# Kernel optimization log

Measured on AMD Instinct MI355X. Metric: run time of the kernel, lower is better.

Reference implementation:

```python
import jax, jax.numpy as jnp
import numpy as np

H = 256
L = 2048
OPINION_LIST = jnp.array([19, 20, 21, 33, 34, 35, 41, 42, 43, 44, 45, 46])


def setup_inputs() -> dict:
    key = jax.random.key(0)
    ks = jax.random.split(key, 8)
    B = 8
    opinion_features = jax.random.normal(ks[0], (B, L, H), dtype=jnp.float32)
    text_features = jax.random.normal(ks[1], (B, L, H), dtype=jnp.float32)
    pos_ids = jax.random.randint(ks[2], (B, L), 0, 47)
    scale = 1.0 / np.sqrt(H)
    Wt = jax.random.normal(ks[3], (H, H), dtype=jnp.float32) * scale
    bt = jax.random.normal(ks[4], (H,), dtype=jnp.float32) * scale
    Wo = jax.random.normal(ks[5], (H, H), dtype=jnp.float32) * scale
    wa = jax.random.normal(ks[6], (2 * H,), dtype=jnp.float32) * scale
    ba = jax.random.normal(ks[7], (1,), dtype=jnp.float32) * scale
    return {"opinion_features": opinion_features, "text_features": text_features,
            "pos_ids": pos_ids, "Wt": Wt, "bt": bt, "Wo": Wo, "wa": wa, "ba": ba}


def position_bias(pos_ids):
    # base: 0.5 on diagonal, 1/log2(2+|i-j|) elsewhere  -> (L, L)
    idx = jnp.arange(L)
    dist = jnp.abs(idx[:, None] - idx[None, :]).astype(jnp.float32)
    base = jnp.where(dist == 0, 0.5, 1.0 / jnp.log2(2.0 + dist))
    # per-token column multiplier: 8 if POS tag is an opinion tag else 1 -> (B, L)
    is_op = (pos_ids[..., None] == OPINION_LIST).any(-1)
    mult = jnp.where(is_op, 8.0, 1.0).astype(jnp.float32)
    return base[None, :, :] * mult[:, None, :]  # (B, L, L)


def reference(opinion_features, text_features, pos_ids, Wt, bt, Wo, wa, ba):
    pos_m = position_bias(pos_ids)                      # (B, L, L)
    t = text_features @ Wt.T + bt                       # (B, L, H)
    o = opinion_features @ Wo.T                         # (B, L, H)
    # tanh(concat([t_i, o_j])) @ wa + ba decomposes additively since tanh is elementwise
    st = jnp.tanh(t) @ wa[:H]                           # (B, L)
    so = jnp.tanh(o) @ wa[H:]                           # (B, L)
    scores = (st[:, :, None] + so[:, None, :] + ba[0]) * pos_m  # (B, L, L)
    att = jax.nn.softmax(scores, axis=-1)
    return att @ opinion_features                       # (B, L, H)
```

## Files before the change

kernel.cpp:

```cpp
#include <hip/hip_runtime.h>

#define B_ 8
#define L_ 2048
#define H_ 256

typedef _Float16 half8 __attribute__((ext_vector_type(8)));
typedef _Float16 half4_t __attribute__((ext_vector_type(4)));
typedef float f32x4 __attribute__((ext_vector_type(4)));

__device__ __forceinline__ float fast_tanh(float x) {
    const float e2 = __expf(2.f * x);
    return 1.f - 2.f * __builtin_amdgcn_rcpf(e2 + 1.f);
}

__global__ __launch_bounds__(256, 2) void prep_kernel(
    const float* __restrict__ opin, const float* __restrict__ text,
    const int* __restrict__ pos_ids,
    const float* __restrict__ Wt, const float* __restrict__ bt,
    const float* __restrict__ Wo, const float* __restrict__ wa,
    const float* __restrict__ ba,
    float* __restrict__ ws_st, float2* __restrict__ ws_cm,
    _Float16* __restrict__ vtg)
{
    __shared__ __align__(16) _Float16 a_lds[4][8][512];
    __shared__ __align__(16) _Float16 w_lds[16][512];

    const int tid  = threadIdx.x;
    const int lane = tid & 63;
    const int rg   = tid >> 6;
    const int mat  = blockIdx.x & 1;
    const size_t g0 = (size_t)(blockIdx.x >> 1) * 64;

    const float* __restrict__ src = mat ? opin : text;
    const float* __restrict__ W   = mat ? Wo   : Wt;

    for (int v = 0; v < 16; ++v) {
        const int idx = v * 256 + tid;
        const int row = idx >> 6;
        const int k   = (idx & 63) * 4;
        const float4 f = *(const float4*)(src + (g0 + row) * 256 + k);
        half4_t h = { (_Float16)f.x, (_Float16)f.y, (_Float16)f.z, (_Float16)f.w };
        const int off = ((row & 15) + 16 * ((k >> 3) & 3)) * 8 + (k & 7);
        *(half4_t*)&a_lds[row >> 4][k >> 5][off] = h;
    }
    __syncthreads();

    f32x4 acc[16];
#pragma unroll
    for (int nt = 0; nt < 16; ++nt) acc[nt] = (f32x4){0.f, 0.f, 0.f, 0.f};

    for (int kc = 0; kc < 8; ++kc) {
        for (int p = 0; p < 8; ++p) {
            const int n = p * 32 + (tid >> 3);
            const int k = (tid & 7) * 4;
            const float4 f = *(const float4*)(W + n * 256 + kc * 32 + k);
            half4_t h = { (_Float16)f.x, (_Float16)f.y, (_Float16)f.z, (_Float16)f.w };
            const int off = ((n & 15) + 16 * (k >> 3)) * 8 + (k & 7);
            *(half4_t*)&w_lds[n >> 4][off] = h;
        }
        __syncthreads();
        const half8 afrag = *(const half8*)&a_lds[rg][kc][lane * 8];
#pragma unroll
        for (int nt = 0; nt < 16; ++nt) {
            const half8 bfrag = *(const half8*)&w_lds[nt][lane * 8];
            acc[nt] = __builtin_amdgcn_mfma_f32_16x16x32_f16(afrag, bfrag, acc[nt], 0, 0, 0);
        }
        __syncthreads();
    }

    const int em = lane & 15, q = lane >> 4;
    float rowsum[4] = {0.f, 0.f, 0.f, 0.f};
#pragma unroll
    for (int nt = 0; nt < 16; ++nt) {
        const int col  = nt * 16 + em;
        const float btv = mat ? 0.f : bt[col];
        const float wav = wa[mat * 256 + col];
#pragma unroll
        for (int r = 0; r < 4; ++r)
            rowsum[r] += fast_tanh(acc[nt][r] + btv) * wav;
    }
#pragma unroll
    for (int r = 0; r < 4; ++r) {
        float s = rowsum[r];
        s += __shfl_xor(s, 1, 64);
        s += __shfl_xor(s, 2, 64);
        s += __shfl_xor(s, 4, 64);
        s += __shfl_xor(s, 8, 64);
        if (em == 0) {
            const size_t grow = g0 + rg * 16 + q * 4 + r;
            if (mat == 0) {
                ws_st[grow] = s;
            } else {
                const int p = pos_ids[grow];
                const bool isop = (p==19)|(p==20)|(p==21)|(p==33)|(p==34)|(p==35)|((p>=41)&(p<=46));
                const float mult = isop ? 8.f : 1.f;
                const float c = s + ba[0];
                ws_cm[grow] = make_float2(c * mult, mult);
            }
        }
    }

    if (mat == 1) {
        const int h = tid;
        const size_t b = g0 >> 11;
        const int kcj = (int)((g0 & 2047) >> 6);
        const int kc = h >> 5, kq = (h >> 3) & 3, jh = h & 7;
        _Float16 vals[64];
#pragma unroll
        for (int r = 0; r < 64; ++r)
            vals[r] = a_lds[r >> 4][kc][((r & 15) + 16 * kq) * 8 + jh];
        _Float16* dst = vtg + ((size_t)b * 32 + kcj) * 16384 + h * 8;
#pragma unroll
        for (int w = 0; w < 8; ++w)
            *(half8*)(dst + w * 2048) = *(half8*)&vals[w * 8];
    }
}

__global__ __launch_bounds__(256, 2) void attn_kernel(
    const float* __restrict__ ws_st, const float2* __restrict__ ws_cm,
    const _Float16* __restrict__ vtg, float* __restrict__ out)
{
    __shared__ float t_lds[2048];
    __shared__ __align__(16) _Float16 p_lds[2][2][2][512];
    __shared__ __align__(16) float alpha_lds[2][32];
    __shared__ float z_lds[32];

    const int tid  = threadIdx.x;
    const int lane = tid & 63;
    const int hq   = tid >> 6;
    const int em   = lane & 15;
    const int q4   = lane >> 4;

    const int b  = blockIdx.x & 7;
    const int i0 = (blockIdx.x >> 3) * 32;

    const int row = tid >> 3;
    const int jg  = tid & 7;
    const int gi  = i0 + row;

#pragma unroll
    for (int v = 0; v < 8; ++v) {
        const int d = tid * 8 + v;
        const float bv = (d == 0) ? 0.5f : 1.0f / __log2f(2.f + (float)d);
        t_lds[d] = bv * 1.44269504088896f;
    }

    const float sti = ws_st[b * 2048 + gi];
    const _Float16* __restrict__ vb =
        vtg + ((size_t)b * 32) * 16384 + q4 * 2048 + (hq * 64 + em) * 8;

    f32x4 acc[2][4];
#pragma unroll
    for (int rt = 0; rt < 2; ++rt)
#pragma unroll
        for (int ht = 0; ht < 4; ++ht) acc[rt][ht] = (f32x4){0.f, 0.f, 0.f, 0.f};
    float m_run = -1e30f;
    float zacc  = 0.f;

    f32x4 vbuf[2][4];
#pragma unroll
    for (int ks = 0; ks < 2; ++ks)
#pragma unroll
        for (int ht = 0; ht < 4; ++ht)
            asm volatile("global_load_dwordx4 %0, %1, off"
                         : "=v"(vbuf[ks][ht])
                         : "v"(vb + ks * 8192 + ht * 128));

    __syncthreads();

    for (int kc = 0; kc < 32; ++kc) {
        const int j0  = kc * 64;
        const int buf = kc & 1;

        float s_arr[8];
        float mx = -1e30f;
        {
            const float4* __restrict__ cmp =
                (const float4*)(ws_cm + b * 2048 + j0 + jg * 8);
#pragma unroll
            for (int w = 0; w < 4; ++w) {
                const float4 c4 = cmp[w];
                const int jj = j0 + jg * 8 + w * 2;
                int d0 = gi - jj;     d0 = d0 < 0 ? -d0 : d0;
                int d1 = gi - jj - 1; d1 = d1 < 0 ? -d1 : d1;
                const float s0 = (sti * c4.y + c4.x) * t_lds[d0];
                const float s1 = (sti * c4.w + c4.z) * t_lds[d1];
                s_arr[2 * w]     = s0;
                s_arr[2 * w + 1] = s1;
                mx = fmaxf(mx, fmaxf(s0, s1));
            }
        }
        mx = fmaxf(mx, __shfl_xor(mx, 1, 64));
        mx = fmaxf(mx, __shfl_xor(mx, 2, 64));
        mx = fmaxf(mx, __shfl_xor(mx, 4, 64));

        const float m_new = fmaxf(m_run, mx);
        const float alpha = __builtin_amdgcn_exp2f(m_run - m_new);
        float zl = 0.f;
        half8 pv;
#pragma unroll
        for (int v = 0; v < 8; ++v) {
            const float p = __builtin_amdgcn_exp2f(s_arr[v] - m_new);
            zl += p;
            pv[v] = (_Float16)p;
        }
        zacc  = zacc * alpha + zl;
        m_run = m_new;

        {
            const int kq = jg & 3;
            const int slot = (((row & 15) ^ (kq << 1)) + 16 * kq);
            *(half8*)&p_lds[buf][row >> 4][jg >> 2][slot * 8] = pv;
        }
        if (jg == 0) alpha_lds[buf][row] = alpha;

        __syncthreads();

        {
            const float4 a0 = *(const float4*)&alpha_lds[buf][q4 * 4];
            const float4 a1 = *(const float4*)&alpha_lds[buf][16 + q4 * 4];
            float ar[2][4] = {{a0.x, a0.y, a0.z, a0.w}, {a1.x, a1.y, a1.z, a1.w}};
            bool upd = false;
#pragma unroll
            for (int rt = 0; rt < 2; ++rt)
#pragma unroll
                for (int r = 0; r < 4; ++r) upd |= (ar[rt][r] != 1.f);
            if (__any(upd)) {
#pragma unroll
                for (int rt = 0; rt < 2; ++rt)
#pragma unroll
                    for (int ht = 0; ht < 4; ++ht)
#pragma unroll
                        for (int r = 0; r < 4; ++r)
                            acc[rt][ht][r] *= ar[rt][r];
            }
        }

        asm volatile("s_waitcnt vmcnt(0)" ::: "memory");
        __builtin_amdgcn_sched_barrier(0);

        {
            const int sl8 = ((em ^ (q4 << 1)) + 16 * q4) * 8;
#pragma unroll
            for (int ks = 0; ks < 2; ++ks) {
                const half8 a0 = *(const half8*)&p_lds[buf][0][ks][sl8];
                const half8 a1 = *(const half8*)&p_lds[buf][1][ks][sl8];
#pragma unroll
                for (int ht = 0; ht < 4; ++ht) {
                    const half8 bh = __builtin_bit_cast(half8, vbuf[ks][ht]);
                    acc[0][ht] = __builtin_amdgcn_mfma_f32_16x16x32_f16(a0, bh, acc[0][ht], 0, 0, 0);
                    acc[1][ht] = __builtin_amdgcn_mfma_f32_16x16x32_f16(a1, bh, acc[1][ht], 0, 0, 0);
                }
            }
        }

        if (kc < 31) {
            const _Float16* __restrict__ pnext = vb + (size_t)(kc + 1) * 16384;
#pragma unroll
            for (int ks = 0; ks < 2; ++ks)
#pragma unroll
                for (int ht = 0; ht < 4; ++ht)
                    asm volatile("global_load_dwordx4 %0, %1, off"
                                 : "=v"(vbuf[ks][ht])
                                 : "v"(pnext + ks * 8192 + ht * 128));
        }
    }

    zacc += __shfl_xor(zacc, 1, 64);
    zacc += __shfl_xor(zacc, 2, 64);
    zacc += __shfl_xor(zacc, 4, 64);
    if (jg == 0) z_lds[row] = zacc;
    __syncthreads();

#pragma unroll
    for (int rt = 0; rt < 2; ++rt) {
#pragma unroll
        for (int r = 0; r < 4; ++r) {
            const int orow = rt * 16 + q4 * 4 + r;
            const float rz = 1.f / z_lds[orow];
#pragma unroll
            for (int ht = 0; ht < 4; ++ht)
                out[((size_t)b * 2048 + i0 + orow) * 256 + hq * 64 + ht * 16 + em] =
                    acc[rt][ht][r] * rz;
        }
    }
}

extern "C" void kernel_launch(void* const* d_in, const int* in_sizes, int n_in,
                              void* d_out, int out_size, void* d_ws, size_t ws_size,
                              hipStream_t stream) {
    const float* opin  = (const float*)d_in[0];
    const float* text  = (const float*)d_in[1];
    const int* pos_ids = (const int*)d_in[2];
    const float* Wt    = (const float*)d_in[3];
    const float* bt    = (const float*)d_in[4];
    const float* Wo    = (const float*)d_in[5];
    const float* wa    = (const float*)d_in[6];
    const float* ba    = (const float*)d_in[7];
    float* out         = (float*)d_out;

    float*  ws_st = (float*)d_ws;
    float2* ws_cm = (float2*)((char*)d_ws + 65536);
    _Float16* vtg = (_Float16*)((char*)d_ws + 65536 + 131072);

    prep_kernel<<<512, 256, 0, stream>>>(opin, text, pos_ids, Wt, bt, Wo, wa, ba,
                                         ws_st, ws_cm, vtg);
    attn_kernel<<<512, 256, 0, stream>>>(ws_st, ws_cm, vtg, out);
}
```

Measured before the change: 150.7 us.

## Software-pipeline weight and V loads, stage cm in LDS, overlap scores with MFMA

In the prep kernel, the next weight K-chunk is prefetched into registers while the current one is converted and used, and the weight LDS buffer is doubled so one barrier per chunk is enough. In the attention kernel, the per-batch cm vector is loaded once into LDS instead of being read from global memory every chunk. The V tiles are double-buffered in registers, and the score/softmax computation for the next chunk is placed after the MFMAs of the current chunk, so global latency and score ALU work overlap with matrix math. The cost is more VGPRs and LDS per block, which could lower occupancy, and a wrapped prefetch past the last chunk that loads data it never uses.

```diff
diff --git a/kernel.cpp b/kernel.cpp
--- a/kernel.cpp
+++ b/kernel.cpp
@@ -12,6 +12,12 @@
     const float e2 = __expf(2.f * x);
     return 1.f - 2.f * __builtin_amdgcn_rcpf(e2 + 1.f);
 }
+
+#define PHASE_BARRIER() do {                                   \
+        asm volatile("s_waitcnt lgkmcnt(0)" ::: "memory");     \
+        __builtin_amdgcn_s_barrier();                          \
+        __builtin_amdgcn_sched_barrier(0);                     \
+    } while (0)
 
 __global__ __launch_bounds__(256, 2) void prep_kernel(
     const float* __restrict__ opin, const float* __restrict__ text,
@@ -23,7 +29,7 @@
     _Float16* __restrict__ vtg)
 {
     __shared__ __align__(16) _Float16 a_lds[4][8][512];
-    __shared__ __align__(16) _Float16 w_lds[16][512];
+    __shared__ __align__(16) _Float16 w_lds[2][16][512];
 
     const int tid  = threadIdx.x;
     const int lane = tid & 63;
@@ -33,6 +39,19 @@
 
     const float* __restrict__ src = mat ? opin : text;
     const float* __restrict__ W   = mat ? Wo   : Wt;
+
+    f32x4 wregA[8], wregB[8];
+#define ISSUE_W(DST, KC) do {                                                   \
+        _Pragma("unroll")                                                       \
+        for (int p = 0; p < 8; ++p) {                                           \
+            const float* p_ = W + (p * 32 + (tid >> 3)) * 256 + (KC) * 32 +     \
+                              (tid & 7) * 4;                                    \
+            asm volatile("global_load_dwordx4 %0, %1, off"                      \
+                         : "=v"(DST[p]) : "v"(p_));                             \
+        }                                                                       \
+    } while (0)
+
+    ISSUE_W(wregA, 0);
 
     for (int v = 0; v < 16; ++v) {
         const int idx = v * 256 + tid;
@@ -43,30 +62,38 @@
         const int off = ((row & 15) + 16 * ((k >> 3) & 3)) * 8 + (k & 7);
         *(half4_t*)&a_lds[row >> 4][k >> 5][off] = h;
     }
-    __syncthreads();
+    PHASE_BARRIER();
 
     f32x4 acc[16];
 #pragma unroll
     for (int nt = 0; nt < 16; ++nt) acc[nt] = (f32x4){0.f, 0.f, 0.f, 0.f};
 
-    for (int kc = 0; kc < 8; ++kc) {
+    auto wbody = [&](const int kc, f32x4 (&cur)[8], f32x4 (&nxt)[8]) {
+        asm volatile("s_waitcnt vmcnt(0)" ::: "memory");
+        __builtin_amdgcn_sched_barrier(0);
+        if (kc < 7) ISSUE_W(nxt, kc + 1);
+#pragma unroll
         for (int p = 0; p < 8; ++p) {
             const int n = p * 32 + (tid >> 3);
             const int k = (tid & 7) * 4;
-            const float4 f = *(const float4*)(W + n * 256 + kc * 32 + k);
+            const float4 f = __builtin_bit_cast(float4, cur[p]);
             half4_t h = { (_Float16)f.x, (_Float16)f.y, (_Float16)f.z, (_Float16)f.w };
             const int off = ((n & 15) + 16 * (k >> 3)) * 8 + (k & 7);
-            *(half4_t*)&w_lds[n >> 4][off] = h;
-        }
-        __syncthreads();
+            *(half4_t*)&w_lds[kc & 1][n >> 4][off] = h;
+        }
+        PHASE_BARRIER();
         const half8 afrag = *(const half8*)&a_lds[rg][kc][lane * 8];
 #pragma unroll
         for (int nt = 0; nt < 16; ++nt) {
-            const half8 bfrag = *(const half8*)&w_lds[nt][lane * 8];
+            const half8 bfrag = *(const half8*)&w_lds[kc & 1][nt][lane * 8];
             acc[nt] = __builtin_amdgcn_mfma_f32_16x16x32_f16(afrag, bfrag, acc[nt], 0, 0, 0);
         }
-        __syncthreads();
-    }
+    };
+    for (int kc = 0; kc < 8; kc += 2) {
+        wbody(kc,     wregA, wregB);
+        wbody(kc + 1, wregB, wregA);
+    }
+#undef ISSUE_W
 
     const int em = lane & 15, q = lane >> 4;
     float rowsum[4] = {0.f, 0.f, 0.f, 0.f};
@@ -121,6 +148,7 @@
     const _Float16* __restrict__ vtg, float* __restrict__ out)
 {
     __shared__ float t_lds[2048];
+    __shared__ float cm_lds[4096];
     __shared__ __align__(16) _Float16 p_lds[2][2][2][512];
     __shared__ __align__(16) float alpha_lds[2][32];
     __shared__ float z_lds[32];
@@ -138,16 +166,36 @@
     const int jg  = tid & 7;
     const int gi  = i0 + row;
 
+    const _Float16* __restrict__ vb =
+        vtg + ((size_t)b * 32) * 16384 + q4 * 2048 + (hq * 64 + em) * 8;
+
+    f32x4 vbA[2][4], vbB[2][4];
+#define ISSUE_VB(DST, KC) do {                                                  \
+        const _Float16* p_ = vb + (size_t)((KC) & 31) * 16384;                  \
+        _Pragma("unroll")                                                       \
+        for (int ks = 0; ks < 2; ++ks)                                          \
+        _Pragma("unroll")                                                       \
+        for (int ht = 0; ht < 4; ++ht)                                          \
+            asm volatile("global_load_dwordx4 %0, %1, off"                      \
+                         : "=v"(DST[ks][ht]) : "v"(p_ + ks * 8192 + ht * 128)); \
+    } while (0)
+
+    ISSUE_VB(vbA, 0);
+
 #pragma unroll
     for (int v = 0; v < 8; ++v) {
         const int d = tid * 8 + v;
         const float bv = (d == 0) ? 0.5f : 1.0f / __log2f(2.f + (float)d);
         t_lds[d] = bv * 1.44269504088896f;
     }
+#pragma unroll
+    for (int v = 0; v < 4; ++v) {
+        const int idx = (v * 256 + tid) * 4;
+        *(float4*)&cm_lds[idx] =
+            *(const float4*)((const float*)(ws_cm + b * 2048) + idx);
+    }
 
     const float sti = ws_st[b * 2048 + gi];
-    const _Float16* __restrict__ vb =
-        vtg + ((size_t)b * 32) * 16384 + q4 * 2048 + (hq * 64 + em) * 8;
 
     f32x4 acc[2][4];
 #pragma unroll
@@ -157,38 +205,24 @@
     float m_run = -1e30f;
     float zacc  = 0.f;
 
-    f32x4 vbuf[2][4];
-#pragma unroll
-    for (int ks = 0; ks < 2; ++ks)
-#pragma unroll
-        for (int ht = 0; ht < 4; ++ht)
-            asm volatile("global_load_dwordx4 %0, %1, off"
-                         : "=v"(vbuf[ks][ht])
-                         : "v"(vb + ks * 8192 + ht * 128));
-
-    __syncthreads();
-
-    for (int kc = 0; kc < 32; ++kc) {
-        const int j0  = kc * 64;
-        const int buf = kc & 1;
-
+    PHASE_BARRIER();
+
+    auto scores = [&](const int kc, const int nbuf) {
+        const int j0 = kc * 64;
         float s_arr[8];
         float mx = -1e30f;
-        {
-            const float4* __restrict__ cmp =
-                (const float4*)(ws_cm + b * 2048 + j0 + jg * 8);
-#pragma unroll
-            for (int w = 0; w < 4; ++w) {
-                const float4 c4 = cmp[w];
-                const int jj = j0 + jg * 8 + w * 2;
-                int d0 = gi - jj;     d0 = d0 < 0 ? -d0 : d0;
-                int d1 = gi - jj - 1; d1 = d1 < 0 ? -d1 : d1;
-                const float s0 = (sti * c4.y + c4.x) * t_lds[d0];
-                const float s1 = (sti * c4.w + c4.z) * t_lds[d1];
-                s_arr[2 * w]     = s0;
-                s_arr[2 * w + 1] = s1;
-                mx = fmaxf(mx, fmaxf(s0, s1));
-            }
+        const float* __restrict__ cmp = &cm_lds[(j0 + jg * 8) * 2];
+#pragma unroll
+        for (int w = 0; w < 4; ++w) {
+            const float4 c4 = *(const float4*)(cmp + w * 4);
+            const int jj = j0 + jg * 8 + w * 2;
+            int d0 = gi - jj;     d0 = d0 < 0 ? -d0 : d0;
+            int d1 = gi - jj - 1; d1 = d1 < 0 ? -d1 : d1;
+            const float s0 = (sti * c4.y + c4.x) * t_lds[d0];
+            const float s1 = (sti * c4.w + c4.z) * t_lds[d1];
+            s_arr[2 * w]     = s0;
+            s_arr[2 * w + 1] = s1;
+            mx = fmaxf(mx, fmaxf(s0, s1));
         }
         mx = fmaxf(mx, __shfl_xor(mx, 1, 64));
         mx = fmaxf(mx, __shfl_xor(mx, 2, 64));
@@ -207,64 +241,68 @@
         zacc  = zacc * alpha + zl;
         m_run = m_new;
 
-        {
-            const int kq = jg & 3;
-            const int slot = (((row & 15) ^ (kq << 1)) + 16 * kq);
-            *(half8*)&p_lds[buf][row >> 4][jg >> 2][slot * 8] = pv;
-        }
-        if (jg == 0) alpha_lds[buf][row] = alpha;
-
-        __syncthreads();
-
-        {
-            const float4 a0 = *(const float4*)&alpha_lds[buf][q4 * 4];
-            const float4 a1 = *(const float4*)&alpha_lds[buf][16 + q4 * 4];
-            float ar[2][4] = {{a0.x, a0.y, a0.z, a0.w}, {a1.x, a1.y, a1.z, a1.w}};
-            bool upd = false;
+        const int kq = jg & 3;
+        const int slot = (((row & 15) ^ (kq << 1)) + 16 * kq);
+        *(half8*)&p_lds[nbuf][row >> 4][jg >> 2][slot * 8] = pv;
+        if (jg == 0) alpha_lds[nbuf][row] = alpha;
+    };
+
+    auto rescale = [&](const int cbuf) {
+        const float4 a0 = *(const float4*)&alpha_lds[cbuf][q4 * 4];
+        const float4 a1 = *(const float4*)&alpha_lds[cbuf][16 + q4 * 4];
+        const float ar[2][4] = {{a0.x, a0.y, a0.z, a0.w}, {a1.x, a1.y, a1.z, a1.w}};
+        bool upd = false;
+#pragma unroll
+        for (int rt = 0; rt < 2; ++rt)
+#pragma unroll
+            for (int r = 0; r < 4; ++r) upd |= (ar[rt][r] != 1.f);
+        if (__any(upd)) {
 #pragma unroll
             for (int rt = 0; rt < 2; ++rt)
 #pragma unroll
-                for (int r = 0; r < 4; ++r) upd |= (ar[rt][r] != 1.f);
-            if (__any(upd)) {
-#pragma unroll
-                for (int rt = 0; rt < 2; ++rt)
-#pragma unroll
-                    for (int ht = 0; ht < 4; ++ht)
-#pragma unroll
-                        for (int r = 0; r < 4; ++r)
-                            acc[rt][ht][r] *= ar[rt][r];
+                for (int ht = 0; ht < 4; ++ht)
+#pragma unroll
+                    for (int r = 0; r < 4; ++r)
+                        acc[rt][ht][r] *= ar[rt][r];
+        }
+    };
+
+    auto mfma_step = [&](const int cbuf, f32x4 (&vbuf)[2][4]) {
+        const int sl8 = ((em ^ (q4 << 1)) + 16 * q4) * 8;
+#pragma unroll
+        for (int ks = 0; ks < 2; ++ks) {
+            const half8 a0 = *(const half8*)&p_lds[cbuf][0][ks][sl8];
+            const half8 a1 = *(const half8*)&p_lds[cbuf][1][ks][sl8];
+#pragma unroll
+            for (int ht = 0; ht < 4; ++ht) {
+                const half8 bh = __builtin_bit_cast(half8, vbuf[ks][ht]);
+                acc[0][ht] = __builtin_amdgcn_mfma_f32_16x16x32_f16(a0, bh, acc[0][ht], 0, 0, 0);
+                acc[1][ht] = __builtin_amdgcn_mfma_f32_16x16x32_f16(a1, bh, acc[1][ht], 0, 0, 0);
             }
         }
-
-        asm volatile("s_waitcnt vmcnt(0)" ::: "memory");
+    };
+
+    scores(0, 0);
+    PHASE_BARRIER();
+
+    for (int kc = 0; kc < 32; kc += 2) {
+        ISSUE_VB(vbB, kc + 1);
+        rescale(0);
+        asm volatile("s_waitcnt vmcnt(8)" ::: "memory");
         __builtin_amdgcn_sched_barrier(0);
-
-        {
-            const int sl8 = ((em ^ (q4 << 1)) + 16 * q4) * 8;
-#pragma unroll
-            for (int ks = 0; ks < 2; ++ks) {
-                const half8 a0 = *(const half8*)&p_lds[buf][0][ks][sl8];
-                const half8 a1 = *(const half8*)&p_lds[buf][1][ks][sl8];
-#pragma unroll
-                for (int ht = 0; ht < 4; ++ht) {
-                    const half8 bh = __builtin_bit_cast(half8, vbuf[ks][ht]);
-                    acc[0][ht] = __builtin_amdgcn_mfma_f32_16x16x32_f16(a0, bh, acc[0][ht], 0, 0, 0);
-                    acc[1][ht] = __builtin_amdgcn_mfma_f32_16x16x32_f16(a1, bh, acc[1][ht], 0, 0, 0);
-                }
-            }
-        }
-
-        if (kc < 31) {
-            const _Float16* __restrict__ pnext = vb + (size_t)(kc + 1) * 16384;
-#pragma unroll
-            for (int ks = 0; ks < 2; ++ks)
-#pragma unroll
-                for (int ht = 0; ht < 4; ++ht)
-                    asm volatile("global_load_dwordx4 %0, %1, off"
-                                 : "=v"(vbuf[ks][ht])
-                                 : "v"(pnext + ks * 8192 + ht * 128));
-        }
-    }
+        mfma_step(0, vbA);
+        scores(kc + 1, 1);
+        PHASE_BARRIER();
+
+        ISSUE_VB(vbA, kc + 2);
+        rescale(1);
+        asm volatile("s_waitcnt vmcnt(8)" ::: "memory");
+        __builtin_amdgcn_sched_barrier(0);
+        mfma_step(1, vbB);
+        if (kc + 2 < 32) scores(kc + 2, 0);
+        PHASE_BARRIER();
+    }
+#undef ISSUE_VB
 
     zacc += __shfl_xor(zacc, 1, 64);
     zacc += __shfl_xor(zacc, 2, 64);
```

After: 139.6 us. 7.3% less time.
